# Performance work log

Measured on AMD Instinct MI355X. Metric: run time of the kernel, lower is better.

The kernel has to match this reference:

```python
import jax, jax.numpy as jnp
import numpy as np

BATCH, T, N_STATE, N_CTRL = 16, 512, 64, 32


def setup_inputs() -> dict:
    key = jax.random.key(0)
    ks = jax.random.split(key, 6)
    n, m = N_STATE, N_CTRL
    # SPD per-step cost: Q = M M^T/(n+m) + I  (guarantees Q_uu invertible)
    M = jax.random.normal(ks[0], (BATCH, T, n + m, n + m), jnp.float32)
    Q = jnp.einsum('btij,btkj->btik', M, M) / (n + m) + jnp.eye(n + m, dtype=jnp.float32)
    p = jax.random.normal(ks[1], (BATCH, T, n + m), jnp.float32)
    # near-stable dynamics so the T-step rollout stays bounded
    A = 0.9 * jnp.eye(n, dtype=jnp.float32) + 0.02 * jax.random.normal(ks[2], (BATCH, T, n, n), jnp.float32)
    B = 0.1 * jax.random.normal(ks[3], (BATCH, T, n, m), jnp.float32)
    c1 = 0.1 * jax.random.normal(ks[4], (BATCH, T, n), jnp.float32)
    x_init = jax.random.normal(ks[5], (BATCH, n), jnp.float32)
    return {'Q': Q, 'p': p, 'A': A, 'B': B, 'c1': c1, 'x_init': x_init}


def _lqr(Q, p, A, B, c1, x_init):
    n = A.shape[-1]
    F = jnp.concatenate([A, B], axis=-1)                      # [b,T,n,n+m]
    # time-major for scan
    Qs = jnp.moveaxis(Q, 1, 0)
    ps = jnp.moveaxis(p, 1, 0)
    Fs = jnp.moveaxis(F, 1, 0)
    cs = jnp.moveaxis(c1, 1, 0)
    bsz = x_init.shape[0]
    V0 = jnp.zeros((bsz, n, n), Q.dtype)
    v0 = jnp.zeros((bsz, n), Q.dtype)

    def bstep(carry, inp):
        V, v = carry
        Qt, pt, Ft, ct = inp
        FtV = jnp.einsum('bij,bik->bjk', Ft, V)               # F^T V : [b,n+m,n]
        Qh = Qt + FtV @ Ft                                     # Q_t + F^T V F
        qh = pt + jnp.einsum('bij,bi->bj', Ft,
                             jnp.einsum('bij,bj->bi', V, ct) + v)
        Quu, Qux = Qh[:, n:, n:], Qh[:, n:, :n]
        Qxx, Qxu = Qh[:, :n, :n], Qh[:, :n, n:]
        qx, qu = qh[:, :n], qh[:, n:]
        L = jnp.linalg.cholesky(Quu)
        rhs = jnp.concatenate([Qux, qu[..., None]], axis=-1)   # solve K and k together
        sol = -jax.scipy.linalg.cho_solve((L, True), rhs)
        K, k = sol[..., :n], sol[..., n]
        QuuK = Quu @ K
        Vn = Qxx + Qxu @ K + jnp.einsum('bji,bjk->bik', K, Qux + QuuK)
        Vn = 0.5 * (Vn + jnp.swapaxes(Vn, -1, -2))             # keep symmetric
        vn = qx + jnp.einsum('bij,bj->bi', Qxu, k) \
             + jnp.einsum('bji,bj->bi', K, qu + jnp.einsum('bij,bj->bi', Quu, k))
        return (Vn, vn), (K, k)

    _, (Ks, ks) = jax.lax.scan(bstep, (V0, v0), (Qs, ps, Fs, cs), reverse=True)

    def fstep(x, inp):
        Kt, kt, At, Bt, ct = inp
        u = jnp.einsum('bij,bj->bi', Kt, x) + kt
        xn = jnp.einsum('bij,bj->bi', At, x) + jnp.einsum('bij,bj->bi', Bt, u) + ct
        return xn, (x, u)

    _, (xs, us) = jax.lax.scan(fstep, x_init,
                               (Ks, ks, jnp.moveaxis(A, 1, 0), jnp.moveaxis(B, 1, 0), cs))
    tau = jnp.concatenate([xs, us], axis=-1)                   # [T,b,n+m]
    return jnp.moveaxis(tau, 0, 1)                             # [b,T,n+m]


def reference(Q, p, A, B, c1, x_init):
    return _lqr(Q, p, A, B, c1, x_init)
```

## Files before the change

### kernel.cpp

```cpp
#include <hip/hip_runtime.h>
#include <math.h>

#define TT 512
#define NB 16

#define QH_B   0
#define LI_B   38400
#define T1_B   43008
#define VBH_B  52368
#define VBL_B  61584
#define FTH_B  70800
#define FTL_B  84624
#define WTH_B  98448
#define WTL_B  112272
#define VR_B   98448
#define XUH_B  126096
#define XUL_B  131216
#define KTH_B  136336
#define KTL_B  141456
#define QHF_B  146576
#define VV_B   146960
#define CV_B   147216
#define KV_B   147472
#define SMB    147600

#define AB0 0
#define AB1 6400
#define KF0 12800
#define KF1 14976
#define XB0 17152
#define XB1 17216
#define UBO 17280
#define AXO 17312

#define WSK_STRIDE 2080

typedef __attribute__((ext_vector_type(8))) short s8v;
typedef __attribute__((ext_vector_type(4))) float f4v;

__device__ __forceinline__ float lanebc(float x, int lane) {
    return __int_as_float(__builtin_amdgcn_readlane(__float_as_int(x), lane));
}
__device__ __forceinline__ float dot4(float4 a, float4 b) {
    return a.x * b.x + a.y * b.y + a.z * b.z + a.w * b.w;
}
__device__ __forceinline__ unsigned short f2bf(float x) {
    unsigned int u = __float_as_uint(x);
    u += 0x7FFFu + ((u >> 16) & 1u);
    return (unsigned short)(u >> 16);
}
__device__ __forceinline__ float bf2f(unsigned short h) {
    return __uint_as_float(((unsigned int)h) << 16);
}
__device__ __forceinline__ void tileMN(int T, int& mt, int& nt) {
    mt = (T >= 15) ? 5 : (T >= 10) ? 4 : (T >= 6) ? 3 : (T >= 3) ? 2 : (T >= 1) ? 1 : 0;
    nt = T - mt * (mt + 1) / 2;
}
#define MFMA(a,b,c) __builtin_amdgcn_mfma_f32_16x16x32_bf16((a),(b),(c),0,0,0)

__launch_bounds__(512, 2)
__global__ void lqr_kernel(const float* __restrict__ Q, const float* __restrict__ P,
                           const float* __restrict__ A, const float* __restrict__ B,
                           const float* __restrict__ c1, const float* __restrict__ xinit,
                           float* __restrict__ out, float* __restrict__ ws)
{
    __shared__ __align__(16) unsigned char smb[SMB];
    float*          QHf = (float*)(smb + QH_B);
    float*          LIf = (float*)(smb + LI_B);
    float*          T1f = (float*)(smb + T1_B);
    unsigned short* VBH = (unsigned short*)(smb + VBH_B);
    unsigned short* VBL = (unsigned short*)(smb + VBL_B);
    unsigned short* FTH = (unsigned short*)(smb + FTH_B);
    unsigned short* FTL = (unsigned short*)(smb + FTL_B);
    unsigned short* WTH = (unsigned short*)(smb + WTH_B);
    unsigned short* WTL = (unsigned short*)(smb + WTL_B);
    float*          VRW = (float*)(smb + VR_B);
    unsigned short* XUH = (unsigned short*)(smb + XUH_B);
    unsigned short* XUL = (unsigned short*)(smb + XUL_B);
    unsigned short* KTH = (unsigned short*)(smb + KTH_B);
    unsigned short* KTL = (unsigned short*)(smb + KTL_B);
    float*          QHF = (float*)(smb + QHF_B);
    float*          VVf = (float*)(smb + VV_B);
    float*          CVf = (float*)(smb + CV_B);
    float*          KVf = (float*)(smb + KV_B);

    const int tid = threadIdx.x;
    const int b   = blockIdx.x;
    const int wv  = tid >> 6;
    const int ln  = tid & 63;
    const int l15 = ln & 15;
    const int lq  = ln >> 4;
    float* wsK = ws;

    const int qcnt = (wv < 5) ? 3 : 2;
    const int qr = ln >> 2, qc4 = ln & 3;

    float4 qreg[3];
    {
        const float* Qg = Q + ((size_t)b * TT + (TT - 1)) * 9216;
        for (int tt = 0; tt < qcnt; ++tt) {
            int T = wv + 8 * tt, mt, nt; tileMN(T, mt, nt);
            qreg[tt] = *(const float4*)&Qg[(16 * mt + qr) * 96 + 16 * nt + 4 * qc4];
        }
    }

    if (tid < 384) {
        const size_t bt = (size_t)b * TT + (TT - 1);
        const int kk = tid & 63, cq = tid >> 6;
#pragma unroll
        for (int q = 0; q < 4; ++q) {
            const float* src = (cq < 4) ? (A + (bt * 64 + kk) * 64 + 16 * cq + 4 * q)
                                        : (B + (bt * 64 + kk) * 32 + 16 * (cq - 4) + 4 * q);
            float4 v = *(const float4*)src;
#pragma unroll
            for (int e = 0; e < 4; ++e) {
                int col = 16 * cq + 4 * q + e;
                float x = (e == 0) ? v.x : (e == 1) ? v.y : (e == 2) ? v.z : v.w;
                unsigned short h = f2bf(x);
                FTH[col * 72 + kk] = h;
                FTL[col * 72 + kk] = f2bf(x - bf2f(h));
            }
        }
    } else {
        float* vb = (float*)VBH;
        for (int i = tid - 384; i < 4608; i += 128) vb[i] = 0.0f;
        if (tid >= 448) VVf[tid - 448] = 0.0f;
    }
    __syncthreads();

    for (int t = TT - 1; t >= 0; --t) {
        const size_t bt  = (size_t)b * TT + t;
        const size_t btp = (size_t)b * TT + ((t > 0) ? (t - 1) : 0);

        for (int tt = 0; tt < qcnt; ++tt) {
            int T = wv + 8 * tt, mt, nt; tileMN(T, mt, nt);
            *(float4*)&QHf[(16 * mt + qr) * 100 + 16 * nt + 4 * qc4] = qreg[tt];
        }
        {
            const float* Qg = Q + btp * 9216;
            for (int tt = 0; tt < qcnt; ++tt) {
                int T = wv + 8 * tt, mt, nt; tileMN(T, mt, nt);
                qreg[tt] = *(const float4*)&Qg[(16 * mt + qr) * 96 + 16 * nt + 4 * qc4];
            }
        }
        float4 fp4[4];
        if (wv >= 1 && wv <= 6) {
            const int tau = tid - 64, kk = tau & 63, cq = tau >> 6;
#pragma unroll
            for (int q = 0; q < 4; ++q) {
                const float* src = (cq < 4) ? (A + (btp * 64 + kk) * 64 + 16 * cq + 4 * q)
                                            : (B + (btp * 64 + kk) * 32 + 16 * (cq - 4) + 4 * q);
                fp4[q] = *(const float4*)src;
            }
        }
        if (wv == 7 && ln < 16)
            *(float4*)&CVf[4 * ln] = *(const float4*)&c1[bt * 64 + 4 * ln];
        float pv = 0.0f;
        if (ln < 48 && (ln & 3) == 0) pv = P[bt * 96 + 12 * wv + (ln >> 2)];

        {
#pragma unroll
            for (int tt = 0; tt < 3; ++tt) {
                int T = wv * 3 + tt, mt = T >> 2, nt = T & 3;
                const unsigned short* ah = FTH + (16 * mt + l15) * 72 + 8 * lq;
                const unsigned short* al = FTL + (16 * mt + l15) * 72 + 8 * lq;
                const unsigned short* bh = VBH + (16 * nt + l15) * 72 + 8 * lq;
                const unsigned short* bl = VBL + (16 * nt + l15) * 72 + 8 * lq;
                f4v d = {0.0f, 0.0f, 0.0f, 0.0f};
#pragma unroll
                for (int kc = 0; kc < 2; ++kc) {
                    s8v Ah = *(const s8v*)(ah + 32 * kc);
                    s8v Al = *(const s8v*)(al + 32 * kc);
                    s8v Bh = *(const s8v*)(bh + 32 * kc);
                    s8v Bl = *(const s8v*)(bl + 32 * kc);
                    d = MFMA(Ah, Bh, d);
                    d = MFMA(Ah, Bl, d);
                    d = MFMA(Al, Bh, d);
                }
                int orow = 16 * mt + 4 * lq, ocol = 16 * nt + l15;
#pragma unroll
                for (int rr = 0; rr < 4; ++rr) {
                    float x = d[rr];
                    unsigned short h = f2bf(x);
                    WTH[(orow + rr) * 72 + ocol] = h;
                    WTL[(orow + rr) * 72 + ocol] = f2bf(x - bf2f(h));
                }
            }
            if (ln < 48) {
                int row = 12 * wv + (ln >> 2), kq = ln & 3;
                float acc = 0.0f;
                const unsigned short* fh = FTH + row * 72 + 16 * kq;
                const unsigned short* fl = FTL + row * 72 + 16 * kq;
                const float* vvp = VVf + 16 * kq;
#pragma unroll
                for (int k = 0; k < 16; ++k)
                    acc += (bf2f(fh[k]) + bf2f(fl[k])) * vvp[k];
                acc += __shfl_xor(acc, 1);
                acc += __shfl_xor(acc, 2);
                if ((ln & 3) == 0) QHF[row] = acc + pv;
            }
        }
        __syncthreads();

        {
            for (int tt = 0; tt < qcnt; ++tt) {
                int T = wv + 8 * tt, mt, nt; tileMN(T, mt, nt);
                int orow = 16 * mt + 4 * lq, ocol = 16 * nt + l15;
                const unsigned short* ah = FTH + (16 * mt + l15) * 72 + 8 * lq;
                const unsigned short* al = FTL + (16 * mt + l15) * 72 + 8 * lq;
                const unsigned short* bh = WTH + (16 * nt + l15) * 72 + 8 * lq;
                const unsigned short* bl = WTL + (16 * nt + l15) * 72 + 8 * lq;
                f4v d;
#pragma unroll
                for (int rr = 0; rr < 4; ++rr)
                    d[rr] = QHf[(orow + rr) * 100 + ocol];
#pragma unroll
                for (int kc = 0; kc < 2; ++kc) {
                    s8v Ah = *(const s8v*)(ah + 32 * kc);
                    s8v Al = *(const s8v*)(al + 32 * kc);
                    s8v Bh = *(const s8v*)(bh + 32 * kc);
                    s8v Bl = *(const s8v*)(bl + 32 * kc);
                    d = MFMA(Ah, Bh, d);
                    d = MFMA(Ah, Bl, d);
                    d = MFMA(Al, Bh, d);
                }
#pragma unroll
                for (int rr = 0; rr < 4; ++rr)
                    QHf[(orow + rr) * 100 + ocol] = d[rr];
                if (mt > nt) {
#pragma unroll
                    for (int rr = 0; rr < 4; ++rr)
                        QHf[ocol * 100 + orow + rr] = d[rr];
                }
                if (mt >= 4 && nt < 4) {
#pragma unroll
                    for (int rr = 0; rr < 4; ++rr) {
                        float x = d[rr];
                        unsigned short h = f2bf(x);
                        XUH[ocol * 40 + (orow + rr - 64)] = h;
                        XUL[ocol * 40 + (orow + rr - 64)] = f2bf(x - bf2f(h));
                    }
                }
            }
        }
        __syncthreads();

        if (wv == 0) {
            const int i = ln & 31;
            float a[32], rinv[32];
#pragma unroll
            for (int j4 = 0; j4 < 8; ++j4) {
                float4 v = *(const float4*)&QHf[(64 + i) * 100 + 64 + 4 * j4];
                a[4 * j4] = v.x; a[4 * j4 + 1] = v.y; a[4 * j4 + 2] = v.z; a[4 * j4 + 3] = v.w;
            }
#pragma unroll
            for (int j = 0; j < 32; ++j) {
                float dj = lanebc(a[j], j);
                float rj = rsqrtf(dj);
                rinv[j] = rj;
                a[j] *= rj;
#pragma unroll
                for (int k = j + 1; k < 32; ++k)
                    a[k] -= a[j] * lanebc(a[j], k);
            }
            float y[32];
#pragma unroll
            for (int r = 0; r < 32; ++r) {
                float acc0 = (r == i) ? 1.0f : 0.0f, acc1 = 0.0f;
#pragma unroll
                for (int j = 0; j < r; ++j) {
                    float lrj = lanebc(a[j], r);
                    if (j & 1) acc1 -= lrj * y[j]; else acc0 -= lrj * y[j];
                }
                y[r] = (acc0 + acc1) * rinv[r];
            }
            if (ln < 32) {
#pragma unroll
                for (int r = 0; r < 32; ++r) LIf[r * 36 + ln] = y[r];
            }
        } else if (wv == 7) {
#pragma unroll
            for (int pass = 0; pass < 2; ++pass) {
                int j = pass ? (64 + (ln & 31)) : ln;
                if (pass && ln >= 32) break;
                float acc = QHF[j];
                const unsigned short* wh = WTH + j * 72;
                const unsigned short* wl = WTL + j * 72;
#pragma unroll 4
                for (int i = 0; i < 64; ++i)
                    acc += (bf2f(wh[i]) + bf2f(wl[i])) * CVf[i];
                QHf[j * 100 + 96] = acc;
            }
        } else {
            const int tau = tid - 64, kk = tau & 63, cq = tau >> 6;
#pragma unroll
            for (int q = 0; q < 4; ++q) {
                float4 v = fp4[q];
#pragma unroll
                for (int e = 0; e < 4; ++e) {
                    int col = 16 * cq + 4 * q + e;
                    float x = (e == 0) ? v.x : (e == 1) ? v.y : (e == 2) ? v.z : v.w;
                    unsigned short h = f2bf(x);
                    FTH[col * 72 + kk] = h;
                    FTL[col * 72 + kk] = f2bf(x - bf2f(h));
                }
            }
        }
        __syncthreads();

        {
            const int c = tid & 63, rq = tid >> 6;
            f4v acc = {0.0f, 0.0f, 0.0f, 0.0f};
#pragma unroll
            for (int j4 = 0; j4 < 8; ++j4) {
                float4 qv = *(const float4*)&QHf[c * 100 + 64 + 4 * j4];
#pragma unroll
                for (int rr = 0; rr < 4; ++rr) {
                    float4 li = *(const float4*)&LIf[(4 * rq + rr) * 36 + 4 * j4];
                    acc[rr] += dot4(li, qv);
                }
            }
            *(f4v*)&T1f[c * 36 + 4 * rq] = acc;
            if (tid < 32) {
                float aq = 0.0f;
#pragma unroll 4
                for (int j = 0; j < 32; ++j)
                    aq += LIf[tid * 36 + j] * QHf[(64 + j) * 100 + 96];
                T1f[64 * 36 + tid] = aq;
            }
        }
        __syncthreads();

        {
            const int c = tid & 63, jq = tid >> 6;
            f4v acc = {0.0f, 0.0f, 0.0f, 0.0f};
#pragma unroll
            for (int i4 = 0; i4 < 8; ++i4) {
                float4 tv = *(const float4*)&T1f[c * 36 + 4 * i4];
#pragma unroll
                for (int ii = 0; ii < 4; ++ii) {
                    float4 li = *(const float4*)&LIf[(4 * i4 + ii) * 36 + 4 * jq];
                    float tvi = (ii == 0) ? tv.x : (ii == 1) ? tv.y : (ii == 2) ? tv.z : tv.w;
                    acc[0] += tvi * li.x; acc[1] += tvi * li.y;
                    acc[2] += tvi * li.z; acc[3] += tvi * li.w;
                }
            }
            float* wrow = wsK + bt * WSK_STRIDE;
#pragma unroll
            for (int jj = 0; jj < 4; ++jj) {
                float kval = -acc[jj];
                unsigned short h = f2bf(kval);
                KTH[c * 40 + 4 * jq + jj] = h;
                KTL[c * 40 + 4 * jq + jj] = f2bf(kval - bf2f(h));
                wrow[(4 * jq + jj) * 65 + c] = kval;
            }
            if (tid < 32) {
                float aq = 0.0f;
#pragma unroll 4
                for (int i = 0; i < 32; ++i)
                    aq += LIf[i * 36 + tid] * T1f[64 * 36 + i];
                KVf[tid] = -aq;
                wsK[bt * WSK_STRIDE + tid * 65 + 64] = -aq;
            }
        }
        __syncthreads();

        {
#pragma unroll
            for (int tt = 0; tt < 2; ++tt) {
                int T = 2 * wv + tt, mt = T >> 2, nt = T & 3;
                int orow = 16 * mt + 4 * lq, ocol = 16 * nt + l15;
                f4v d;
#pragma unroll
                for (int rr = 0; rr < 4; ++rr)
                    d[rr] = QHf[(orow + rr) * 100 + ocol];
                s8v Ah = *(const s8v*)(XUH + (16 * mt + l15) * 40 + 8 * lq);
                s8v Al = *(const s8v*)(XUL + (16 * mt + l15) * 40 + 8 * lq);
                s8v Bh = *(const s8v*)(KTH + (16 * nt + l15) * 40 + 8 * lq);
                s8v Bl = *(const s8v*)(KTL + (16 * nt + l15) * 40 + 8 * lq);
                d = MFMA(Ah, Bh, d);
                d = MFMA(Ah, Bl, d);
                d = MFMA(Al, Bh, d);
#pragma unroll
                for (int rr = 0; rr < 4; ++rr)
                    VRW[(orow + rr) * 72 + ocol] = d[rr];
            }
        }
        __syncthreads();

        if (tid < 256) {
            const int rg = tid >> 4, cgv = tid & 15;
            float4 m0[4], m1[4];
#pragma unroll
            for (int rr = 0; rr < 4; ++rr) {
                m0[rr] = *(const float4*)&VRW[(4 * rg + rr) * 72 + 4 * cgv];
                m1[rr] = *(const float4*)&VRW[(4 * cgv + rr) * 72 + 4 * rg];
            }
#pragma unroll
            for (int rr = 0; rr < 4; ++rr) {
                float s[4];
                s[0] = 0.5f * (m0[rr].x + ((float*)&m1[0])[rr]);
                s[1] = 0.5f * (m0[rr].y + ((float*)&m1[1])[rr]);
                s[2] = 0.5f * (m0[rr].z + ((float*)&m1[2])[rr]);
                s[3] = 0.5f * (m0[rr].w + ((float*)&m1[3])[rr]);
                unsigned short h[4], lo[4];
#pragma unroll
                for (int cc = 0; cc < 4; ++cc) {
                    h[cc]  = f2bf(s[cc]);
                    lo[cc] = f2bf(s[cc] - bf2f(h[cc]));
                }
                ushort4 hv = make_ushort4(h[0], h[1], h[2], h[3]);
                ushort4 lv = make_ushort4(lo[0], lo[1], lo[2], lo[3]);
                *(ushort4*)&VBH[(4 * rg + rr) * 72 + 4 * cgv] = hv;
                *(ushort4*)&VBL[(4 * rg + rr) * 72 + 4 * cgv] = lv;
            }
        } else if (tid < 320) {
            const int r = tid & 63;
            float acc = QHf[r * 100 + 96];
#pragma unroll
            for (int j4 = 0; j4 < 8; ++j4) {
                float4 qv = *(const float4*)&QHf[r * 100 + 64 + 4 * j4];
                float4 kv = *(const float4*)&KVf[4 * j4];
                acc += dot4(qv, kv);
            }
            VVf[r] = acc;
        }
        __syncthreads();
    }

    float* sm = (float*)smb;
    {
        const size_t bt0 = (size_t)b * TT;
#pragma unroll
        for (int it = 0; it < 3; ++it) {
            int q = tid + 512 * it, row = q / 24, g = q % 24;
            const float* src = (g < 16) ? (A + (bt0 * 64 + row) * 64 + 4 * g)
                                        : (B + (bt0 * 64 + row) * 32 + 4 * (g - 16));
            *(float4*)&sm[AB0 + row * 100 + 4 * g] = *(const float4*)src;
        }
#pragma unroll
        for (int i = 0; i < 5; ++i) {
            int idx = tid + 512 * i;
            if (idx < 2080) {
                int j = idx / 65, c = idx - 65 * j;
                sm[KF0 + j * 68 + c] = wsK[bt0 * WSK_STRIDE + idx];
            }
        }
        if (tid < 64) sm[XB0 + tid] = xinit[b * 64 + tid];
    }
    __syncthreads();

    for (int t = 0; t < TT; ++t) {
        const size_t bt  = (size_t)b * TT + t;
        const size_t btn = (size_t)b * TT + ((t < TT - 1) ? (t + 1) : t);
        const int cur = t & 1;
        const int abC = cur ? AB1 : AB0, abN = cur ? AB0 : AB1;
        const int kfC = cur ? KF1 : KF0, kfN = cur ? KF0 : KF1;
        const int xbC = cur ? XB1 : XB0, xbN = cur ? XB0 : XB1;

        float4 abpre[6];
        float kpre[9];
        float cpre = 0.0f;
        if (tid >= 256) {
            const int t2 = tid - 256;
#pragma unroll
            for (int it = 0; it < 6; ++it) {
                int q = t2 + 256 * it, row = q / 24, g = q % 24;
                const float* src = (g < 16) ? (A + (btn * 64 + row) * 64 + 4 * g)
                                            : (B + (btn * 64 + row) * 32 + 4 * (g - 16));
                abpre[it] = *(const float4*)src;
            }
#pragma unroll
            for (int i = 0; i < 9; ++i) {
                int idx = t2 + 256 * i;
                kpre[i] = (idx < 2080) ? wsK[btn * WSK_STRIDE + idx] : 0.0f;
            }
            cpre = c1[bt * 64 + ((tid - 256) >> 2)];
        }

        if (tid < 256) {
            const int j = tid >> 3, q = tid & 7;
            float4 k0 = *(const float4*)&sm[kfC + j * 68 + 8 * q];
            float4 k1 = *(const float4*)&sm[kfC + j * 68 + 8 * q + 4];
            float4 x0 = *(const float4*)&sm[xbC + 8 * q];
            float4 x1 = *(const float4*)&sm[xbC + 8 * q + 4];
            float pa = dot4(k0, x0) + dot4(k1, x1);
            pa += __shfl_xor(pa, 1);
            pa += __shfl_xor(pa, 2);
            pa += __shfl_xor(pa, 4);
            if (q == 0) {
                float u = pa + sm[kfC + j * 68 + 64];
                sm[UBO + j] = u;
                out[bt * 96 + 64 + j] = u;
            }
        } else {
            const int r = (tid - 256) >> 2, q = tid & 3;
            float pa = 0.0f;
#pragma unroll
            for (int e4 = 0; e4 < 4; ++e4) {
                float4 av = *(const float4*)&sm[abC + r * 100 + 16 * q + 4 * e4];
                float4 xv = *(const float4*)&sm[xbC + 16 * q + 4 * e4];
                pa += dot4(av, xv);
            }
            pa += __shfl_xor(pa, 1);
            pa += __shfl_xor(pa, 2);
            if (q == 0) sm[AXO + r] = pa + cpre;
            if (q == 1) out[bt * 96 + r] = sm[xbC + r];
        }
        __syncthreads();

        if (tid < 256) {
            const int r = tid >> 2, q = tid & 3;
            float4 b0 = *(const float4*)&sm[abC + r * 100 + 64 + 8 * q];
            float4 b1 = *(const float4*)&sm[abC + r * 100 + 64 + 8 * q + 4];
            float4 u0 = *(const float4*)&sm[UBO + 8 * q];
            float4 u1 = *(const float4*)&sm[UBO + 8 * q + 4];
            float pa = dot4(b0, u0) + dot4(b1, u1);
            pa += __shfl_xor(pa, 1);
            pa += __shfl_xor(pa, 2);
            if (q == 0) sm[xbN + r] = sm[AXO + r] + pa;
        } else {
            const int t2 = tid - 256;
#pragma unroll
            for (int it = 0; it < 6; ++it) {
                int q = t2 + 256 * it, row = q / 24, g = q % 24;
                *(float4*)&sm[abN + row * 100 + 4 * g] = abpre[it];
            }
#pragma unroll
            for (int i = 0; i < 9; ++i) {
                int idx = t2 + 256 * i;
                if (idx < 2080) {
                    int j = idx / 65, c = idx - 65 * j;
                    sm[kfN + j * 68 + c] = kpre[i];
                }
            }
        }
        __syncthreads();
    }
}

extern "C" void kernel_launch(void* const* d_in, const int* in_sizes, int n_in,
                              void* d_out, int out_size, void* d_ws, size_t ws_size,
                              hipStream_t stream) {
    (void)in_sizes; (void)n_in; (void)out_size;
    const float* Q  = (const float*)d_in[0];
    const float* p  = (const float*)d_in[1];
    const float* A  = (const float*)d_in[2];
    const float* B  = (const float*)d_in[3];
    const float* c1 = (const float*)d_in[4];
    const float* xi = (const float*)d_in[5];
    if (ws_size < (size_t)NB * TT * WSK_STRIDE * sizeof(float)) return;
    lqr_kernel<<<NB, 512, 0, stream>>>(Q, p, A, B, c1, xi, (float*)d_out, (float*)d_ws);
}
```

Before: 9.074 ms.

## Rebalance backward-step phases, drop symmetrization pass and one barrier per step

Splits the Qh tile MFMA work across two phases so the Cholesky wave runs concurrently with the remaining tile products, and moves the F-matrix bf16 split conversion into a later phase with a flattened load pattern. The separate V symmetrization pass through a float scratch buffer and its barrier are removed; V is written directly as hi/lo bf16 from the MFMA result, and the v update becomes a shuffle-reduced parallel dot product. This cuts one sync and one LDS round trip per time step, but drops the explicit symmetrization, which may let asymmetric rounding error accumulate. It also replaces the stored reciprocal pivots with rcp of the broadcast diagonal.

```diff
diff --git a/kernel.cpp b/kernel.cpp
--- a/kernel.cpp
+++ b/kernel.cpp
@@ -13,7 +13,6 @@
 #define FTL_B  84624
 #define WTH_B  98448
 #define WTL_B  112272
-#define VR_B   98448
 #define XUH_B  126096
 #define XUL_B  131216
 #define KTH_B  136336
@@ -74,7 +73,6 @@
     unsigned short* FTL = (unsigned short*)(smb + FTL_B);
     unsigned short* WTH = (unsigned short*)(smb + WTH_B);
     unsigned short* WTL = (unsigned short*)(smb + WTL_B);
-    float*          VRW = (float*)(smb + VR_B);
     unsigned short* XUH = (unsigned short*)(smb + XUH_B);
     unsigned short* XUL = (unsigned short*)(smb + XUL_B);
     unsigned short* KTH = (unsigned short*)(smb + KTH_B);
@@ -98,7 +96,8 @@
     float4 qreg[3];
     {
         const float* Qg = Q + ((size_t)b * TT + (TT - 1)) * 9216;
-        for (int tt = 0; tt < qcnt; ++tt) {
+#pragma unroll
+        for (int tt = 0; tt < 3; ++tt) if (tt < qcnt) {
             int T = wv + 8 * tt, mt, nt; tileMN(T, mt, nt);
             qreg[tt] = *(const float4*)&Qg[(16 * mt + qr) * 96 + 16 * nt + 4 * qc4];
         }
@@ -132,31 +131,76 @@
         const size_t bt  = (size_t)b * TT + t;
         const size_t btp = (size_t)b * TT + ((t > 0) ? (t - 1) : 0);
 
-        for (int tt = 0; tt < qcnt; ++tt) {
+#pragma unroll
+        for (int tt = 0; tt < 3; ++tt) if (tt < qcnt) {
             int T = wv + 8 * tt, mt, nt; tileMN(T, mt, nt);
             *(float4*)&QHf[(16 * mt + qr) * 100 + 16 * nt + 4 * qc4] = qreg[tt];
         }
         {
             const float* Qg = Q + btp * 9216;
-            for (int tt = 0; tt < qcnt; ++tt) {
+#pragma unroll
+            for (int tt = 0; tt < 3; ++tt) if (tt < qcnt) {
                 int T = wv + 8 * tt, mt, nt; tileMN(T, mt, nt);
                 qreg[tt] = *(const float4*)&Qg[(16 * mt + qr) * 96 + 16 * nt + 4 * qc4];
             }
         }
         float4 fp4[4];
-        if (wv >= 1 && wv <= 6) {
-            const int tau = tid - 64, kk = tau & 63, cq = tau >> 6;
-#pragma unroll
-            for (int q = 0; q < 4; ++q) {
-                const float* src = (cq < 4) ? (A + (btp * 64 + kk) * 64 + 16 * cq + 4 * q)
-                                            : (B + (btp * 64 + kk) * 32 + 16 * (cq - 4) + 4 * q);
-                fp4[q] = *(const float4*)src;
+        if (tid >= 64) {
+#pragma unroll
+            for (int it = 0; it < 4; ++it) {
+                int idx = (tid - 64) + 448 * it;
+                if (idx < 1536) {
+                    int kk = idx / 24, g = idx % 24;
+                    const float* src = (g < 16) ? (A + (btp * 64 + kk) * 64 + 4 * g)
+                                                : (B + (btp * 64 + kk) * 32 + 4 * (g - 16));
+                    fp4[it] = *(const float4*)src;
+                }
             }
         }
         if (wv == 7 && ln < 16)
             *(float4*)&CVf[4 * ln] = *(const float4*)&c1[bt * 64 + 4 * ln];
         float pv = 0.0f;
         if (ln < 48 && (ln & 3) == 0) pv = P[bt * 96 + 12 * wv + (ln >> 2)];
+
+        auto qhTile = [&](int T) {
+            int mt, nt; tileMN(T, mt, nt);
+            int orow = 16 * mt + 4 * lq, ocol = 16 * nt + l15;
+            const unsigned short* ah = FTH + (16 * mt + l15) * 72 + 8 * lq;
+            const unsigned short* al = FTL + (16 * mt + l15) * 72 + 8 * lq;
+            const unsigned short* bh = WTH + (16 * nt + l15) * 72 + 8 * lq;
+            const unsigned short* bl = WTL + (16 * nt + l15) * 72 + 8 * lq;
+            f4v d;
+#pragma unroll
+            for (int rr = 0; rr < 4; ++rr)
+                d[rr] = QHf[(orow + rr) * 100 + ocol];
+#pragma unroll
+            for (int kc = 0; kc < 2; ++kc) {
+                s8v Ah = *(const s8v*)(ah + 32 * kc);
+                s8v Al = *(const s8v*)(al + 32 * kc);
+                s8v Bh = *(const s8v*)(bh + 32 * kc);
+                s8v Bl = *(const s8v*)(bl + 32 * kc);
+                d = MFMA(Ah, Bh, d);
+                d = MFMA(Ah, Bl, d);
+                d = MFMA(Al, Bh, d);
+            }
+#pragma unroll
+            for (int rr = 0; rr < 4; ++rr)
+                QHf[(orow + rr) * 100 + ocol] = d[rr];
+            if (mt > nt) {
+#pragma unroll
+                for (int rr = 0; rr < 4; ++rr)
+                    QHf[ocol * 100 + orow + rr] = d[rr];
+            }
+            if (mt >= 4 && nt < 4) {
+#pragma unroll
+                for (int rr = 0; rr < 4; ++rr) {
+                    float x = d[rr];
+                    unsigned short h = f2bf(x);
+                    XUH[ocol * 40 + (orow + rr - 64)] = h;
+                    XUL[ocol * 40 + (orow + rr - 64)] = f2bf(x - bf2f(h));
+                }
+            }
+        };
 
         {
 #pragma unroll
@@ -203,51 +247,16 @@
         __syncthreads();
 
         {
-            for (int tt = 0; tt < qcnt; ++tt) {
-                int T = wv + 8 * tt, mt, nt; tileMN(T, mt, nt);
-                int orow = 16 * mt + 4 * lq, ocol = 16 * nt + l15;
-                const unsigned short* ah = FTH + (16 * mt + l15) * 72 + 8 * lq;
-                const unsigned short* al = FTL + (16 * mt + l15) * 72 + 8 * lq;
-                const unsigned short* bh = WTH + (16 * nt + l15) * 72 + 8 * lq;
-                const unsigned short* bl = WTL + (16 * nt + l15) * 72 + 8 * lq;
-                f4v d;
-#pragma unroll
-                for (int rr = 0; rr < 4; ++rr)
-                    d[rr] = QHf[(orow + rr) * 100 + ocol];
-#pragma unroll
-                for (int kc = 0; kc < 2; ++kc) {
-                    s8v Ah = *(const s8v*)(ah + 32 * kc);
-                    s8v Al = *(const s8v*)(al + 32 * kc);
-                    s8v Bh = *(const s8v*)(bh + 32 * kc);
-                    s8v Bl = *(const s8v*)(bl + 32 * kc);
-                    d = MFMA(Ah, Bh, d);
-                    d = MFMA(Ah, Bl, d);
-                    d = MFMA(Al, Bh, d);
-                }
-#pragma unroll
-                for (int rr = 0; rr < 4; ++rr)
-                    QHf[(orow + rr) * 100 + ocol] = d[rr];
-                if (mt > nt) {
-#pragma unroll
-                    for (int rr = 0; rr < 4; ++rr)
-                        QHf[ocol * 100 + orow + rr] = d[rr];
-                }
-                if (mt >= 4 && nt < 4) {
-#pragma unroll
-                    for (int rr = 0; rr < 4; ++rr) {
-                        float x = d[rr];
-                        unsigned short h = f2bf(x);
-                        XUH[ocol * 40 + (orow + rr - 64)] = h;
-                        XUL[ocol * 40 + (orow + rr - 64)] = f2bf(x - bf2f(h));
-                    }
-                }
-            }
+            int T = (wv == 0) ? 14 : (wv == 1) ? 19 : (wv == 2) ? 20 :
+                    (wv == 3) ? 0  : (wv == 4) ? 1  : (wv == 5) ? 2  :
+                    (wv == 6) ? 3  : 4;
+            qhTile(T);
         }
         __syncthreads();
 
         if (wv == 0) {
             const int i = ln & 31;
-            float a[32], rinv[32];
+            float a[32];
 #pragma unroll
             for (int j4 = 0; j4 < 8; ++j4) {
                 float4 v = *(const float4*)&QHf[(64 + i) * 100 + 64 + 4 * j4];
@@ -257,7 +266,6 @@
             for (int j = 0; j < 32; ++j) {
                 float dj = lanebc(a[j], j);
                 float rj = rsqrtf(dj);
-                rinv[j] = rj;
                 a[j] *= rj;
 #pragma unroll
                 for (int k = j + 1; k < 32; ++k)
@@ -272,37 +280,32 @@
                     float lrj = lanebc(a[j], r);
                     if (j & 1) acc1 -= lrj * y[j]; else acc0 -= lrj * y[j];
                 }
-                y[r] = (acc0 + acc1) * rinv[r];
+                y[r] = (acc0 + acc1) * __builtin_amdgcn_rcpf(lanebc(a[r], r));
             }
             if (ln < 32) {
 #pragma unroll
                 for (int r = 0; r < 32; ++r) LIf[r * 36 + ln] = y[r];
             }
-        } else if (wv == 7) {
-#pragma unroll
-            for (int pass = 0; pass < 2; ++pass) {
-                int j = pass ? (64 + (ln & 31)) : ln;
-                if (pass && ln >= 32) break;
-                float acc = QHF[j];
-                const unsigned short* wh = WTH + j * 72;
-                const unsigned short* wl = WTL + j * 72;
+        } else {
+            const int Ta = (wv == 1) ? 5 : (wv == 2) ? 7 : (wv == 3) ? 9 :
+                           (wv == 4) ? 11 : (wv == 5) ? 13 : (wv == 6) ? 16 : 18;
+            qhTile(Ta);
+            if (wv <= 6) {
+                const int Tb = (wv == 1) ? 6 : (wv == 2) ? 8 : (wv == 3) ? 10 :
+                               (wv == 4) ? 12 : (wv == 5) ? 15 : 17;
+                qhTile(Tb);
+            } else {
+#pragma unroll
+                for (int pass = 0; pass < 2; ++pass) {
+                    int j = pass ? (64 + (ln & 31)) : ln;
+                    if (pass && ln >= 32) break;
+                    float acc = QHF[j];
+                    const unsigned short* wh = WTH + j * 72;
+                    const unsigned short* wl = WTL + j * 72;
 #pragma unroll 4
-                for (int i = 0; i < 64; ++i)
-                    acc += (bf2f(wh[i]) + bf2f(wl[i])) * CVf[i];
-                QHf[j * 100 + 96] = acc;
-            }
-        } else {
-            const int tau = tid - 64, kk = tau & 63, cq = tau >> 6;
-#pragma unroll
-            for (int q = 0; q < 4; ++q) {
-                float4 v = fp4[q];
-#pragma unroll
-                for (int e = 0; e < 4; ++e) {
-                    int col = 16 * cq + 4 * q + e;
-                    float x = (e == 0) ? v.x : (e == 1) ? v.y : (e == 2) ? v.z : v.w;
-                    unsigned short h = f2bf(x);
-                    FTH[col * 72 + kk] = h;
-                    FTL[col * 72 + kk] = f2bf(x - bf2f(h));
+                    for (int i = 0; i < 64; ++i)
+                        acc += (bf2f(wh[i]) + bf2f(wl[i])) * CVf[i];
+                    QHf[j * 100 + 96] = acc;
                 }
             }
         }
@@ -327,6 +330,24 @@
                 for (int j = 0; j < 32; ++j)
                     aq += LIf[tid * 36 + j] * QHf[(64 + j) * 100 + 96];
                 T1f[64 * 36 + tid] = aq;
+            }
+            if (tid >= 64) {
+#pragma unroll
+                for (int it = 0; it < 4; ++it) {
+                    int idx = (tid - 64) + 448 * it;
+                    if (idx < 1536) {
+                        int kk = idx / 24, g = idx % 24;
+                        float4 v = fp4[it];
+#pragma unroll
+                        for (int e = 0; e < 4; ++e) {
+                            int col = 4 * g + e;
+                            float x = (e == 0) ? v.x : (e == 1) ? v.y : (e == 2) ? v.z : v.w;
+                            unsigned short h = f2bf(x);
+                            FTH[col * 72 + kk] = h;
+                            FTL[col * 72 + kk] = f2bf(x - bf2f(h));
+                        }
+                    }
+                }
             }
         }
         __syncthreads();
@@ -382,48 +403,26 @@
                 d = MFMA(Ah, Bl, d);
                 d = MFMA(Al, Bh, d);
 #pragma unroll
-                for (int rr = 0; rr < 4; ++rr)
-                    VRW[(orow + rr) * 72 + ocol] = d[rr];
-            }
-        }
-        __syncthreads();
-
-        if (tid < 256) {
-            const int rg = tid >> 4, cgv = tid & 15;
-            float4 m0[4], m1[4];
-#pragma unroll
-            for (int rr = 0; rr < 4; ++rr) {
-                m0[rr] = *(const float4*)&VRW[(4 * rg + rr) * 72 + 4 * cgv];
-                m1[rr] = *(const float4*)&VRW[(4 * cgv + rr) * 72 + 4 * rg];
-            }
-#pragma unroll
-            for (int rr = 0; rr < 4; ++rr) {
-                float s[4];
-                s[0] = 0.5f * (m0[rr].x + ((float*)&m1[0])[rr]);
-                s[1] = 0.5f * (m0[rr].y + ((float*)&m1[1])[rr]);
-                s[2] = 0.5f * (m0[rr].z + ((float*)&m1[2])[rr]);
-                s[3] = 0.5f * (m0[rr].w + ((float*)&m1[3])[rr]);
-                unsigned short h[4], lo[4];
-#pragma unroll
-                for (int cc = 0; cc < 4; ++cc) {
-                    h[cc]  = f2bf(s[cc]);
-                    lo[cc] = f2bf(s[cc] - bf2f(h[cc]));
-                }
-                ushort4 hv = make_ushort4(h[0], h[1], h[2], h[3]);
-                ushort4 lv = make_ushort4(lo[0], lo[1], lo[2], lo[3]);
-                *(ushort4*)&VBH[(4 * rg + rr) * 72 + 4 * cgv] = hv;
-                *(ushort4*)&VBL[(4 * rg + rr) * 72 + 4 * cgv] = lv;
-            }
-        } else if (tid < 320) {
-            const int r = tid & 63;
-            float acc = QHf[r * 100 + 96];
-#pragma unroll
-            for (int j4 = 0; j4 < 8; ++j4) {
-                float4 qv = *(const float4*)&QHf[r * 100 + 64 + 4 * j4];
-                float4 kv = *(const float4*)&KVf[4 * j4];
-                acc += dot4(qv, kv);
-            }
-            VVf[r] = acc;
+                for (int rr = 0; rr < 4; ++rr) {
+                    float x = d[rr];
+                    unsigned short h = f2bf(x);
+                    VBH[(orow + rr) * 72 + ocol] = h;
+                    VBL[(orow + rr) * 72 + ocol] = f2bf(x - bf2f(h));
+                }
+            }
+            {
+                int r = 8 * wv + (ln >> 3), kq = ln & 7;
+                float acc = 0.0f;
+#pragma unroll
+                for (int e = 0; e < 4; ++e) {
+                    int j = 4 * kq + e;
+                    acc += QHf[r * 100 + 64 + j] * KVf[j];
+                }
+                acc += __shfl_xor(acc, 1);
+                acc += __shfl_xor(acc, 2);
+                acc += __shfl_xor(acc, 4);
+                if (kq == 0) VVf[r] = acc + QHf[r * 100 + 96];
+            }
         }
         __syncthreads();
     }
```

Result: slower. 10.61 ms (+16.9%).
